# Kernel tuning notes

Hardware: AMD Instinct MI355X
Metric: run time of the kernel (lower is better)

Reference implementation:

```python
import jax, jax.numpy as jnp
import numpy as np

H = 256
B, S = 8, 2048
WIN = 16


def setup_inputs() -> dict:
    key = jax.random.key(0)
    k1, k2, k3, k4, k5 = jax.random.split(key, 5)
    bound = 1.0 / np.sqrt(H)  # torch nn.RNN init range
    x = jax.random.normal(k1, (B, S, H), dtype=jnp.float32)
    W_ih = jax.random.uniform(k2, (H, H), jnp.float32, -bound, bound)
    W_hh = jax.random.uniform(k3, (H, H), jnp.float32, -bound, bound)
    b_ih = jax.random.uniform(k4, (H,), jnp.float32, -bound, bound)
    b_hh = jax.random.uniform(k5, (H,), jnp.float32, -bound, bound)
    return {"x": x, "W_ih": W_ih, "W_hh": W_hh, "b_ih": b_ih, "b_hh": b_hh, "window": WIN}


def reference(x, W_ih, W_hh, b_ih, b_hh, window):
    # Original: get_K builds [B, S, window, H] overlapping windows (left-padded
    # with window-1 zeros), runs an RNN over each length-`window` sequence with
    # h0 = 0, and keeps the last hidden state -> [B, S, H].
    # Equivalent streaming form: at step k of the window, every position t
    # consumes xpad[:, t + k]; so slice a shifted view of the padded input and
    # update all B*S hidden states at once (never materializing the windows).
    b, s, h = x.shape
    xpad = jnp.pad(x, ((0, 0), (window - 1, 0), (0, 0)))  # [B, S+W-1, H]

    def step(hid, k):
        xk = jax.lax.dynamic_slice(xpad, (0, k, 0), (b, s, h))  # [B, S, H]
        hid = jnp.tanh(xk @ W_ih.T + b_ih + hid @ W_hh.T + b_hh)
        return hid, None

    h0 = jnp.zeros((b, s, h), dtype=x.dtype)
    h_last, _ = jax.lax.scan(step, h0, jnp.arange(window))
    return h_last  # [B, S, H]
```

## Files before the change

### kernel.cpp

```cpp
#include <hip/hip_runtime.h>

#define HDIM 256
#define SEQ 2048

typedef _Float16 half8_t __attribute__((ext_vector_type(8)));
typedef float floatx16 __attribute__((ext_vector_type(16)));

#define U_PITCH 1024
#define H_PITCH 512
#define U_ROWS 79
#define HA0_OFF (U_ROWS * U_PITCH)
#define LDS_BYTES (HA0_OFF + 65536)

static __device__ __forceinline__ float exp2f_fast(float x) {
  float r; asm("v_exp_f32 %0, %1" : "=v"(r) : "v"(x)); return r;
}
static __device__ __forceinline__ float rcpf_fast(float x) {
  float r; asm("v_rcp_f32 %0, %1" : "=v"(r) : "v"(x)); return r;
}
static __device__ __forceinline__ float tanhf_fast(float x) {
  float e = exp2f_fast(x * 2.8853900817779268f);
  return 1.0f - 2.0f * rcpf_fast(e + 1.0f);
}
static __device__ __forceinline__ unsigned pkh(float a, float b) {
  return __builtin_bit_cast(unsigned, __builtin_amdgcn_cvt_pkrtz(a, b));
}

__global__ __launch_bounds__(512, 1) void winrnn_kernel(
    const float* __restrict__ x, const float* __restrict__ W_ih,
    const float* __restrict__ W_hh, const float* __restrict__ b_ih,
    const float* __restrict__ b_hh, float* __restrict__ out) {
  extern __shared__ char smem[];
  const int tid = threadIdx.x;
  const int w = tid >> 6;
  const int lane = tid & 63;
  const int l31 = lane & 31;
  const int hi = lane >> 5;

  const int wg = blockIdx.x;
  const int batch = wg >> 5;
  const int t0 = (wg & 31) * 64;
  const float* xb = x + (size_t)batch * SEQ * HDIM;

  const int t = w & 1;
  const int jbase = (w >> 1) * 64;
  const int tb = t * 32;
  const int hswz = l31 << 4;
  char* const hbuf = smem + HA0_OFF + t * 32768;

  {
    char* xl = smem + HA0_OFF;
#pragma unroll
    for (int it = 0; it < 12; ++it) {
      int idx = tid + it * 512;
      int row = idx >> 6;
      int c4 = idx & 63;
      int xi = t0 - 15 + row;
      float4 v = make_float4(0.f, 0.f, 0.f, 0.f);
      if (row < U_ROWS && xi >= 0)
        v = *reinterpret_cast<const float4*>(xb + (size_t)xi * HDIM + c4 * 4);
      uint2 u;
      u.x = pkh(v.x, v.y);
      u.y = pkh(v.z, v.w);
      *reinterpret_cast<uint2*>(xl + row * H_PITCH + ((c4 * 8) ^ ((row & 31) << 4))) = u;
    }
  }

  half8_t Wf[2][16];
#pragma unroll
  for (int jt = 0; jt < 2; ++jt)
#pragma unroll
    for (int kt = 0; kt < 16; ++kt) {
      const float* wp = W_ih + (size_t)(jbase + jt * 32 + l31) * HDIM + kt * 16 + hi * 8;
      float4 a = *reinterpret_cast<const float4*>(wp);
      float4 b = *reinterpret_cast<const float4*>(wp + 4);
      uint4 uu;
      uu.x = pkh(a.x, a.y); uu.y = pkh(a.z, a.w);
      uu.z = pkh(b.x, b.y); uu.w = pkh(b.z, b.w);
      Wf[jt][kt] = __builtin_bit_cast(half8_t, uu);
    }

  float4 biasf[2][4];
#pragma unroll
  for (int jt = 0; jt < 2; ++jt)
#pragma unroll
    for (int g = 0; g < 4; ++g) {
      int j0 = jbase + jt * 32 + g * 8 + hi * 4;
      float4 bi = *reinterpret_cast<const float4*>(b_ih + j0);
      float4 bh = *reinterpret_cast<const float4*>(b_hh + j0);
      biasf[jt][g] = make_float4(bi.x + bh.x, bi.y + bh.y, bi.z + bh.z, bi.w + bh.w);
    }

  __syncthreads();

  {
    const char* xl = smem + HA0_OFF;
    char* Ul = smem;
    for (int s = t; s < 3; s += 2) {
      int prow = s * 32 + l31;
      floatx16 acc0, acc1;
#pragma unroll
      for (int g = 0; g < 4; ++g) {
        acc0[4*g+0] = biasf[0][g].x; acc0[4*g+1] = biasf[0][g].y;
        acc0[4*g+2] = biasf[0][g].z; acc0[4*g+3] = biasf[0][g].w;
        acc1[4*g+0] = biasf[1][g].x; acc1[4*g+1] = biasf[1][g].y;
        acc1[4*g+2] = biasf[1][g].z; acc1[4*g+3] = biasf[1][g].w;
      }
#pragma unroll
      for (int kt = 0; kt < 16; ++kt) {
        half8_t xB = *reinterpret_cast<const half8_t*>(
            xl + prow * H_PITCH + ((kt * 32 + hi * 16) ^ ((prow & 31) << 4)));
        acc0 = __builtin_amdgcn_mfma_f32_32x32x16_f16(Wf[0][kt], xB, acc0, 0, 0, 0);
        acc1 = __builtin_amdgcn_mfma_f32_32x32x16_f16(Wf[1][kt], xB, acc1, 0, 0, 0);
      }
      if (prow < U_ROWS) {
        int uswz = (prow & 31) << 4;
#pragma unroll
        for (int jt = 0; jt < 2; ++jt)
#pragma unroll
          for (int g = 0; g < 4; ++g) {
            const floatx16& ac = jt ? acc1 : acc0;
            int j0 = jbase + jt * 32 + g * 8 + hi * 4;
            float4 st;
            st.x = ac[4*g+0]; st.y = ac[4*g+1]; st.z = ac[4*g+2]; st.w = ac[4*g+3];
            *reinterpret_cast<float4*>(Ul + prow * U_PITCH + ((j0 * 4) ^ uswz)) = st;
          }
      }
    }
  }

#pragma unroll
  for (int jt = 0; jt < 2; ++jt)
#pragma unroll
    for (int kt = 0; kt < 16; ++kt) {
      const float* wp = W_hh + (size_t)(jbase + jt * 32 + l31) * HDIM + kt * 16 + hi * 8;
      float4 a = *reinterpret_cast<const float4*>(wp);
      float4 b = *reinterpret_cast<const float4*>(wp + 4);
      uint4 uu;
      uu.x = pkh(a.x, a.y); uu.y = pkh(a.z, a.w);
      uu.z = pkh(b.x, b.y); uu.w = pkh(b.z, b.w);
      Wf[jt][kt] = __builtin_bit_cast(half8_t, uu);
    }

  __syncthreads();

  const char* Ul = smem;
  floatx16 acc0, acc0b, acc1, acc1b;

  for (int k = 0; k < 16; ++k) {
    {
      const int urow = tb + l31 + k;
      const int uswz = (urow & 31) << 4;
#pragma unroll
      for (int g = 0; g < 4; ++g) {
        int j00 = (jbase + g * 8 + hi * 4) * 4;
        float4 u0 = *reinterpret_cast<const float4*>(Ul + urow * U_PITCH + (j00 ^ uswz));
        float4 u1 = *reinterpret_cast<const float4*>(Ul + urow * U_PITCH + ((j00 + 128) ^ uswz));
        acc0[4*g+0] = u0.x; acc0[4*g+1] = u0.y; acc0[4*g+2] = u0.z; acc0[4*g+3] = u0.w;
        acc1[4*g+0] = u1.x; acc1[4*g+1] = u1.y; acc1[4*g+2] = u1.z; acc1[4*g+3] = u1.w;
        acc0b[4*g+0] = 0.f; acc0b[4*g+1] = 0.f; acc0b[4*g+2] = 0.f; acc0b[4*g+3] = 0.f;
        acc1b[4*g+0] = 0.f; acc1b[4*g+1] = 0.f; acc1b[4*g+2] = 0.f; acc1b[4*g+3] = 0.f;
      }
    }
    if (k > 0) {
      const char* hr = hbuf + ((k & 1) ? 0 : 16384);
#pragma unroll
      for (int kt = 0; kt < 8; ++kt) {
        int off0 = (kt * 32 + hi * 16) ^ hswz;
        int off1 = ((kt + 8) * 32 + hi * 16) ^ hswz;
        half8_t h0 = *reinterpret_cast<const half8_t*>(hr + l31 * H_PITCH + off0);
        half8_t h1 = *reinterpret_cast<const half8_t*>(hr + l31 * H_PITCH + off1);
        acc0  = __builtin_amdgcn_mfma_f32_32x32x16_f16(Wf[0][kt],     h0, acc0,  0, 0, 0);
        acc0b = __builtin_amdgcn_mfma_f32_32x32x16_f16(Wf[0][kt + 8], h1, acc0b, 0, 0, 0);
        acc1  = __builtin_amdgcn_mfma_f32_32x32x16_f16(Wf[1][kt],     h0, acc1,  0, 0, 0);
        acc1b = __builtin_amdgcn_mfma_f32_32x32x16_f16(Wf[1][kt + 8], h1, acc1b, 0, 0, 0);
      }
    }
    if (k < 15) {
      char* hw = hbuf + ((k & 1) ? 16384 : 0);
#pragma unroll
      for (int g = 0; g < 4; ++g) {
        float a0 = tanhf_fast(acc0[4*g+0] + acc0b[4*g+0]);
        float a1 = tanhf_fast(acc0[4*g+1] + acc0b[4*g+1]);
        float a2 = tanhf_fast(acc0[4*g+2] + acc0b[4*g+2]);
        float a3 = tanhf_fast(acc0[4*g+3] + acc0b[4*g+3]);
        float b0 = tanhf_fast(acc1[4*g+0] + acc1b[4*g+0]);
        float b1 = tanhf_fast(acc1[4*g+1] + acc1b[4*g+1]);
        float b2 = tanhf_fast(acc1[4*g+2] + acc1b[4*g+2]);
        float b3 = tanhf_fast(acc1[4*g+3] + acc1b[4*g+3]);
        int jb = (jbase + g * 8 + hi * 4) * 2;
        uint2 u0; u0.x = pkh(a0, a1); u0.y = pkh(a2, a3);
        uint2 u1; u1.x = pkh(b0, b1); u1.y = pkh(b2, b3);
        *reinterpret_cast<uint2*>(hw + l31 * H_PITCH + (jb ^ hswz)) = u0;
        *reinterpret_cast<uint2*>(hw + l31 * H_PITCH + ((jb + 64) ^ hswz)) = u1;
      }
      __syncthreads();
    }
  }
  acc0 += acc0b;
  acc1 += acc1b;

  __syncthreads();
  {
    char* ol = smem + HA0_OFF;
    const int orow = tb + l31;
    const int oswz = (orow & 31) << 4;
#pragma unroll
    for (int jt = 0; jt < 2; ++jt) {
      const floatx16& ac = jt ? acc1 : acc0;
#pragma unroll
      for (int g = 0; g < 4; ++g) {
        float4 st;
        st.x = tanhf_fast(ac[4*g+0]); st.y = tanhf_fast(ac[4*g+1]);
        st.z = tanhf_fast(ac[4*g+2]); st.w = tanhf_fast(ac[4*g+3]);
        int jb4 = (jbase + jt * 32 + g * 8 + hi * 4) * 4;
        *reinterpret_cast<float4*>(ol + orow * 1024 + (jb4 ^ oswz)) = st;
      }
    }
  }
  __syncthreads();
  {
    const char* ol = smem + HA0_OFF;
    float* ob = out + ((size_t)batch * SEQ + t0) * HDIM;
#pragma unroll
    for (int it = 0; it < 8; ++it) {
      int idx = tid + it * 512;
      int row = idx >> 6;
      int c = idx & 63;
      float4 v = *reinterpret_cast<const float4*>(
          ol + row * 1024 + ((c * 16) ^ ((row & 31) << 4)));
      *reinterpret_cast<float4*>(ob + (size_t)row * HDIM + c * 4) = v;
    }
  }
}

extern "C" void kernel_launch(void* const* d_in, const int* in_sizes, int n_in,
                              void* d_out, int out_size, void* d_ws, size_t ws_size,
                              hipStream_t stream) {
  const float* x    = (const float*)d_in[0];
  const float* W_ih = (const float*)d_in[1];
  const float* W_hh = (const float*)d_in[2];
  const float* b_ih = (const float*)d_in[3];
  const float* b_hh = (const float*)d_in[4];
  float* out = (float*)d_out;
  static_assert(LDS_BYTES <= 160 * 1024, "LDS budget");
  hipFuncSetAttribute(reinterpret_cast<const void*>(winrnn_kernel),
                      hipFuncAttributeMaxDynamicSharedMemorySize, LDS_BYTES);
  winrnn_kernel<<<dim3(256), dim3(512), LDS_BYTES, stream>>>(x, W_ih, W_hh, b_ih, b_hh, out);
}
```

Measured before the change: 74.07 us.

## Split each workgroup into two 256-thread blocks over 32 positions

Each workgroup now covers 32 sequence positions with 4 waves instead of 64 positions with 8 waves, and the grid doubles to 512 workgroups. LDS per block shrinks so two blocks can share a CU. The aim is to let independent blocks overlap their per-step barriers, tanh work and MFMA latency instead of stalling a whole CU on one barrier. In exchange, the 15-row window halo is recomputed more often: the input projection does 64 rows per 32 positions instead of 96 per 64.

```diff
diff --git a/kernel.cpp b/kernel.cpp
--- a/kernel.cpp
+++ b/kernel.cpp
@@ -2,15 +2,17 @@
 
 #define HDIM 256
 #define SEQ 2048
+#define TPOS 32
 
 typedef _Float16 half8_t __attribute__((ext_vector_type(8)));
 typedef float floatx16 __attribute__((ext_vector_type(16)));
 
 #define U_PITCH 1024
 #define H_PITCH 512
-#define U_ROWS 79
-#define HA0_OFF (U_ROWS * U_PITCH)
-#define LDS_BYTES (HA0_OFF + 65536)
+#define U_ROWS 47
+#define H0_OFF (U_ROWS * U_PITCH)
+#define H1_OFF (H0_OFF + 16384)
+#define LDS_BYTES (H0_OFF + 32768)
 
 static __device__ __forceinline__ float exp2f_fast(float x) {
   float r; asm("v_exp_f32 %0, %1" : "=v"(r) : "v"(x)); return r;
@@ -26,7 +28,7 @@
   return __builtin_bit_cast(unsigned, __builtin_amdgcn_cvt_pkrtz(a, b));
 }
 
-__global__ __launch_bounds__(512, 1) void winrnn_kernel(
+__global__ __launch_bounds__(256, 1) void winrnn_kernel(
     const float* __restrict__ x, const float* __restrict__ W_ih,
     const float* __restrict__ W_hh, const float* __restrict__ b_ih,
     const float* __restrict__ b_hh, float* __restrict__ out) {
@@ -38,31 +40,30 @@
   const int hi = lane >> 5;
 
   const int wg = blockIdx.x;
-  const int batch = wg >> 5;
-  const int t0 = (wg & 31) * 64;
+  const int batch = wg >> 6;
+  const int t0 = (wg & 63) * TPOS;
   const float* xb = x + (size_t)batch * SEQ * HDIM;
 
-  const int t = w & 1;
-  const int jbase = (w >> 1) * 64;
-  const int tb = t * 32;
+  const int jbase = w * 64;
   const int hswz = l31 << 4;
-  char* const hbuf = smem + HA0_OFF + t * 32768;
-
-  {
-    char* xl = smem + HA0_OFF;
+
+  {
+    char* xl = smem + H0_OFF;
 #pragma unroll
     for (int it = 0; it < 12; ++it) {
-      int idx = tid + it * 512;
+      int idx = tid + it * 256;
       int row = idx >> 6;
       int c4 = idx & 63;
       int xi = t0 - 15 + row;
-      float4 v = make_float4(0.f, 0.f, 0.f, 0.f);
-      if (row < U_ROWS && xi >= 0)
-        v = *reinterpret_cast<const float4*>(xb + (size_t)xi * HDIM + c4 * 4);
-      uint2 u;
-      u.x = pkh(v.x, v.y);
-      u.y = pkh(v.z, v.w);
-      *reinterpret_cast<uint2*>(xl + row * H_PITCH + ((c4 * 8) ^ ((row & 31) << 4))) = u;
+      if (row < U_ROWS) {
+        float4 v = make_float4(0.f, 0.f, 0.f, 0.f);
+        if (xi >= 0)
+          v = *reinterpret_cast<const float4*>(xb + (size_t)xi * HDIM + c4 * 4);
+        uint2 u;
+        u.x = pkh(v.x, v.y);
+        u.y = pkh(v.z, v.w);
+        *reinterpret_cast<uint2*>(xl + row * H_PITCH + ((c4 * 8) ^ ((row & 31) << 4))) = u;
+      }
     }
   }
 
@@ -94,9 +95,10 @@
   __syncthreads();
 
   {
-    const char* xl = smem + HA0_OFF;
+    const char* xl = smem + H0_OFF;
     char* Ul = smem;
-    for (int s = t; s < 3; s += 2) {
+#pragma unroll
+    for (int s = 0; s < 2; ++s) {
       int prow = s * 32 + l31;
       floatx16 acc0, acc1;
 #pragma unroll
@@ -145,11 +147,13 @@
   __syncthreads();
 
   const char* Ul = smem;
+  char* hb0 = smem + H0_OFF;
+  char* hb1 = smem + H1_OFF;
   floatx16 acc0, acc0b, acc1, acc1b;
 
   for (int k = 0; k < 16; ++k) {
     {
-      const int urow = tb + l31 + k;
+      const int urow = l31 + k;
       const int uswz = (urow & 31) << 4;
 #pragma unroll
       for (int g = 0; g < 4; ++g) {
@@ -163,7 +167,7 @@
       }
     }
     if (k > 0) {
-      const char* hr = hbuf + ((k & 1) ? 0 : 16384);
+      const char* hr = (k & 1) ? hb0 : hb1;
 #pragma unroll
       for (int kt = 0; kt < 8; ++kt) {
         int off0 = (kt * 32 + hi * 16) ^ hswz;
@@ -177,7 +181,7 @@
       }
     }
     if (k < 15) {
-      char* hw = hbuf + ((k & 1) ? 16384 : 0);
+      char* hw = (k & 1) ? hb1 : hb0;
 #pragma unroll
       for (int g = 0; g < 4; ++g) {
         float a0 = tanhf_fast(acc0[4*g+0] + acc0b[4*g+0]);
@@ -202,9 +206,8 @@
 
   __syncthreads();
   {
-    char* ol = smem + HA0_OFF;
-    const int orow = tb + l31;
-    const int oswz = (orow & 31) << 4;
+    char* ol = smem + H0_OFF;
+    const int oswz = (l31 & 31) << 4;
 #pragma unroll
     for (int jt = 0; jt < 2; ++jt) {
       const floatx16& ac = jt ? acc1 : acc0;
@@ -214,17 +217,17 @@
         st.x = tanhf_fast(ac[4*g+0]); st.y = tanhf_fast(ac[4*g+1]);
         st.z = tanhf_fast(ac[4*g+2]); st.w = tanhf_fast(ac[4*g+3]);
         int jb4 = (jbase + jt * 32 + g * 8 + hi * 4) * 4;
-        *reinterpret_cast<float4*>(ol + orow * 1024 + (jb4 ^ oswz)) = st;
-      }
-    }
-  }
-  __syncthreads();
-  {
-    const char* ol = smem + HA0_OFF;
+        *reinterpret_cast<float4*>(ol + l31 * 1024 + (jb4 ^ oswz)) = st;
+      }
+    }
+  }
+  __syncthreads();
+  {
+    const char* ol = smem + H0_OFF;
     float* ob = out + ((size_t)batch * SEQ + t0) * HDIM;
 #pragma unroll
     for (int it = 0; it < 8; ++it) {
-      int idx = tid + it * 512;
+      int idx = tid + it * 256;
       int row = idx >> 6;
       int c = idx & 63;
       float4 v = *reinterpret_cast<const float4*>(
@@ -243,8 +246,8 @@
   const float* b_ih = (const float*)d_in[3];
   const float* b_hh = (const float*)d_in[4];
   float* out = (float*)d_out;
-  static_assert(LDS_BYTES <= 160 * 1024, "LDS budget");
+  static_assert(2 * LDS_BYTES <= 160 * 1024, "2 WGs/CU capacity");
   hipFuncSetAttribute(reinterpret_cast<const void*>(winrnn_kernel),
                       hipFuncAttributeMaxDynamicSharedMemorySize, LDS_BYTES);
-  winrnn_kernel<<<dim3(256), dim3(512), LDS_BYTES, stream>>>(x, W_ih, W_hh, b_ih, b_hh, out);
-}
+  winrnn_kernel<<<dim3(512), dim3(256), LDS_BYTES, stream>>>(x, W_ih, W_hh, b_ih, b_hh, out);
+}
```

Result: slower. 85.91 us (+16.0%).
